# Performance work log

Hardware: AMD Instinct MI355X
Metric: run time of the kernel (lower is better)

The kernel has to match this reference:

```python
import jax, jax.numpy as jnp
import numpy as np

# Faithful JAX port of FeatureSimilarity(similarity_type='l2'):
#   -(features[:, None, :] - features[None, :, :]).norm(2, dim=-1)
# Implemented via the algebraically-equal expansion ||x-y||^2 = ||x||^2 + ||y||^2 - 2<x,y>
# to avoid materializing the [N, N, D] broadcast intermediate (32 GB at these sizes).

def setup_inputs() -> dict:
    key = jax.random.key(0)
    features = jax.random.normal(key, (8192, 128), dtype=jnp.float32)  # [N, D]
    return {"features": features}

def reference(features):
    sq = jnp.sum(features * features, axis=-1)                     # [N]
    d2 = sq[:, None] + sq[None, :] - 2.0 * (features @ features.T)  # [N, N]
    d2 = jnp.maximum(d2, 0.0)  # clamp tiny negatives from cancellation
    return -jnp.sqrt(d2)
```

## Files before the change

kernel.cpp:

```cpp
#include <hip/hip_runtime.h>
#include <hip/hip_bf16.h>


typedef __attribute__((ext_vector_type(8))) short short8;
typedef __attribute__((ext_vector_type(4))) float float4v;

#define FS_N 8192
#define FS_D 128

static __device__ __forceinline__ unsigned short f32_to_bf16_rne(float x) {
    unsigned u = __float_as_uint(x);
    u += 0x7FFFu + ((u >> 16) & 1u);
    return (unsigned short)(u >> 16);
}
static __device__ __forceinline__ float bf16_to_f32(unsigned short b) {
    return __uint_as_float(((unsigned)b) << 16);
}

__global__ __launch_bounds__(256) void fs_convert_kernel(
        const float* __restrict__ in, unsigned short* __restrict__ fbT,
        float* __restrict__ sq) {
    const int rt = blockIdx.x;
    const int t  = threadIdx.x;
    const int rl = t >> 4;
    const int g  = t & 15;
    const int row = rt * 16 + rl;

    const float4* src = (const float4*)(in + row * FS_D + g * 8);
    const float4 v0 = src[0];
    const float4 v1 = src[1];

    short8 packed;
    float s = 0.0f;
    {
        const float vv[8] = {v0.x, v0.y, v0.z, v0.w, v1.x, v1.y, v1.z, v1.w};
        #pragma unroll
        for (int e = 0; e < 8; ++e) {
            const unsigned short b = f32_to_bf16_rne(vv[e]);
            packed[e] = (short)b;
            const float f = bf16_to_f32(b);
            s += f * f;
        }
    }

    const int ks   = g >> 2;
    const int quad = g & 3;
    short8* dst = (short8*)(fbT + (((size_t)(rt * 4 + ks) * 64) + quad * 16 + rl) * 8);
    *dst = packed;

    #pragma unroll
    for (int off = 8; off > 0; off >>= 1) s += __shfl_xor(s, off);
    if (g == 0) sq[row] = s;
}

__global__ __launch_bounds__(256) void fs_gemm_kernel(
        const unsigned short* __restrict__ fbT, const float* __restrict__ sq,
        float* __restrict__ out) {
    const int ti   = blockIdx.x;
    const int tj   = blockIdx.y;
    const int wid  = threadIdx.x >> 6;
    const int lane = threadIdx.x & 63;
    const int wm   = wid >> 1, wn = wid & 1;
    const int l15  = lane & 15;
    const int quad = lane >> 4;

    const int arow = ti * 128 + wm * 64;
    const int brow = tj * 128 + wn * 64;

    const int rta = ti * 8 + wm * 4;
    const int rtb = tj * 8 + wn * 4;

    float4v acc[4][4];
    #pragma unroll
    for (int m = 0; m < 4; ++m)
        #pragma unroll
        for (int n = 0; n < 4; ++n)
            acc[m][n] = (float4v){0.f, 0.f, 0.f, 0.f};

    #pragma unroll
    for (int ks = 0; ks < 4; ++ks) {
        short8 a[4], b[4];
        #pragma unroll
        for (int m = 0; m < 4; ++m)
            a[m] = *(const short8*)(fbT + (size_t)((rta + m) * 4 + ks) * 512 + lane * 8);
        #pragma unroll
        for (int n = 0; n < 4; ++n)
            b[n] = *(const short8*)(fbT + (size_t)((rtb + n) * 4 + ks) * 512 + lane * 8);
        #pragma unroll
        for (int m = 0; m < 4; ++m)
            #pragma unroll
            for (int n = 0; n < 4; ++n)
                acc[m][n] = __builtin_amdgcn_mfma_f32_16x16x32_bf16(
                    a[m], b[n], acc[m][n], 0, 0, 0);
    }

    #pragma unroll
    for (int n = 0; n < 4; ++n) {
        const int   col = brow + n * 16 + l15;
        const float sqc = sq[col];
        float* outcol = out + (size_t)col * FS_N;
        #pragma unroll
        for (int m = 0; m < 4; ++m) {
            const int rbase = arow + m * 16 + quad * 4;
            const float4v sqr = *(const float4v*)(sq + rbase);
            float4v o;
            #pragma unroll
            for (int r = 0; r < 4; ++r) {
                float d2 = sqr[r] + sqc - 2.0f * acc[m][n][r];
                d2 = fmaxf(d2, 0.0f);
                o[r] = -__builtin_sqrtf(d2);
            }
            __builtin_nontemporal_store(o, (float4v*)(outcol + rbase));
        }
    }
}

extern "C" void kernel_launch(void* const* d_in, const int* in_sizes, int n_in,
                              void* d_out, int out_size, void* d_ws, size_t ws_size,
                              hipStream_t stream) {
    const float* features = (const float*)d_in[0];
    float*       out      = (float*)d_out;

    unsigned short* fbT = (unsigned short*)d_ws;
    float*          sq  = (float*)((char*)d_ws + (size_t)FS_N * FS_D * sizeof(unsigned short));

    fs_convert_kernel<<<FS_N / 16, 256, 0, stream>>>(features, fbT, sq);

    dim3 grid(FS_N / 128, FS_N / 128);
    fs_gemm_kernel<<<grid, 256, 0, stream>>>(fbT, sq, out);
}
```

Before: 288.9 us.

## Exploit symmetry: compute upper-triangle tiles and mirror via LDS transpose

Blocks below the diagonal now exit early. Each upper-triangle block writes its tile as before and also writes the transposed tile to the mirrored location, staged through swizzled shared memory. This roughly halves the MFMA and operand-load work, but the output store volume is unchanged. Nontemporal stores are replaced with normal stores, extra syncthreads and LDS traffic are added, and half the launched blocks sit idle.

```diff
diff --git a/kernel.cpp b/kernel.cpp
--- a/kernel.cpp
+++ b/kernel.cpp
@@ -56,8 +56,12 @@
 __global__ __launch_bounds__(256) void fs_gemm_kernel(
         const unsigned short* __restrict__ fbT, const float* __restrict__ sq,
         float* __restrict__ out) {
-    const int ti   = blockIdx.x;
-    const int tj   = blockIdx.y;
+    const int ti = blockIdx.x;
+    const int tj = blockIdx.y;
+    if (tj < ti) return;
+
+    __shared__ float T[4][2048];
+
     const int wid  = threadIdx.x >> 6;
     const int lane = threadIdx.x & 63;
     const int wm   = wid >> 1, wn = wid & 1;
@@ -110,7 +114,38 @@
                 d2 = fmaxf(d2, 0.0f);
                 o[r] = -__builtin_sqrtf(d2);
             }
-            __builtin_nontemporal_store(o, (float4v*)(outcol + rbase));
+            *(float4v*)(outcol + rbase) = o;
+            acc[m][n] = o;
+        }
+    }
+
+    if (ti == tj) return;
+
+    float* Tw = T[wid];
+    #pragma unroll
+    for (int sp = 0; sp < 2; ++sp) {
+        __syncthreads();
+        #pragma unroll
+        for (int nn = 0; nn < 2; ++nn) {
+            const int n = sp * 2 + nn;
+            #pragma unroll
+            for (int m = 0; m < 4; ++m) {
+                #pragma unroll
+                for (int r = 0; r < 4; ++r) {
+                    const int x  = m * 16 + quad * 4 + r;
+                    const int yy = nn * 16 + l15;
+                    Tw[x * 32 + (yy ^ ((x & 7) << 2))] = acc[m][n][r];
+                }
+            }
+        }
+        __syncthreads();
+        #pragma unroll
+        for (int s = 0; s < 8; ++s) {
+            const int xp   = s * 8 + quad * 2 + (l15 >> 3);
+            const int fidx = xp * 8 + ((l15 & 7) ^ (xp & 7));
+            const float4v o2 = ((const float4v*)Tw)[fidx];
+            *(float4v*)(out + (size_t)(arow + xp) * FS_N
+                            + brow + sp * 32 + (l15 & 7) * 4) = o2;
         }
     }
 }
```

Measured after the change: 284.2 us. No clear change (-1.6%).
